# Optimization experiments

Measured on AMD Instinct MI355X. Metric: run time of the kernel, lower is better.

Reference implementation:

```python
import jax, jax.numpy as jnp
import numpy as np

EPS = 1e-6     # torch F.pairwise_distance eps (added to the difference)
MARGIN = 1.0


def setup_inputs() -> dict:
    key = jax.random.key(0)
    k1, k2, k3 = jax.random.split(key, 3)
    dim = 2400
    anchor = jax.random.normal(k1, (1, dim), dtype=jnp.float32)
    positive_samples = jax.random.normal(k2, (5, dim), dtype=jnp.float32)
    negative_samples = jax.random.normal(k3, (50000, dim), dtype=jnp.float32)
    return {"anchor": anchor, "positive_samples": positive_samples,
            "negative_samples": negative_samples}


def reference(anchor, positive_samples, negative_samples):
    # Faithful to the torch loop: TripletMarginLoss(margin=1.0, p=2, swap=False,
    # reduction='sum') applied to each chunk of num_pos negatives, summed.
    # d(x, y) = ||x - y + eps||_2  (torch pairwise_distance semantics)
    P = positive_samples.shape[0]            # 5 personas
    N = negative_samples.shape[0]
    C = N // P                               # number of full chunks (partial dropped)
    # anchor broadcasts (1, D) against (P, D)
    d_ap = jnp.sqrt(jnp.sum(jnp.square(anchor - positive_samples + EPS), axis=-1))  # (P,)
    neg = negative_samples[: C * P].reshape(C, P, -1)                               # (C, P, D)
    d_an = jnp.sqrt(jnp.sum(jnp.square(anchor[None] - neg + EPS), axis=-1))         # (C, P)
    loss = jnp.sum(jax.nn.relu(d_ap[None, :] - d_an + MARGIN))
    return loss
```

## Files before the change

### kernel.cpp

```cpp
#include <hip/hip_runtime.h>
#include <math.h>

#define DIM 2400
#define VEC (DIM / 4)
#define EPS 1e-6f
#define MARGIN 1.0f
#define NPOS 5

__global__ void dap_kernel(const float* __restrict__ anchor,
                           const float* __restrict__ pos,
                           float* __restrict__ dap,
                           float* __restrict__ out) {
    const int lane = threadIdx.x & 63;
    const int wave = threadIdx.x >> 6;
    const float4* a4 = (const float4*)anchor;
    const float4* p4 = (const float4*)(pos + wave * DIM);

    float acc = 0.0f;
    for (int w = lane; w < VEC; w += 64) {
        float4 a = a4[w];
        float4 b = p4[w];
        float dx = a.x - b.x + EPS;
        float dy = a.y - b.y + EPS;
        float dz = a.z - b.z + EPS;
        float dw = a.w - b.w + EPS;
        acc = fmaf(dx, dx, fmaf(dy, dy, fmaf(dz, dz, fmaf(dw, dw, acc))));
    }
    #pragma unroll
    for (int off = 32; off > 0; off >>= 1)
        acc += __shfl_down(acc, off, 64);
    if (lane == 0) dap[wave] = sqrtf(acc);
    if (threadIdx.x == 0) *out = 0.0f;
}

__global__ __launch_bounds__(256, 4)
void triplet_kernel(const float* __restrict__ anchor,
                    const float* __restrict__ neg,
                    const float* __restrict__ dap,
                    float* __restrict__ out,
                    int n_rows) {
    __shared__ float4 s_anchor[VEC];
    __shared__ float  s_dap[NPOS];
    __shared__ float  s_partial[4];

    for (int i = threadIdx.x; i < VEC; i += blockDim.x)
        s_anchor[i] = ((const float4*)anchor)[i];
    if (threadIdx.x < NPOS)
        s_dap[threadIdx.x] = dap[threadIdx.x];
    __syncthreads();

    const int lane = threadIdx.x & 63;
    const int wave = threadIdx.x >> 6;
    const int waves_per_block = blockDim.x >> 6;
    const int stride = gridDim.x * waves_per_block;

    float local = 0.0f;
    for (int row = blockIdx.x * waves_per_block + wave; row < n_rows; row += stride) {
        const float4* nr = (const float4*)(neg + (size_t)row * DIM);
        float acc = 0.0f;
        #pragma unroll 3
        for (int w = lane; w < VEC; w += 64) {
            float4 a = s_anchor[w];
            float4 b = nr[w];
            float dx = a.x - b.x + EPS;
            float dy = a.y - b.y + EPS;
            float dz = a.z - b.z + EPS;
            float dw = a.w - b.w + EPS;
            acc = fmaf(dx, dx, fmaf(dy, dy, fmaf(dz, dz, fmaf(dw, dw, acc))));
        }
        #pragma unroll
        for (int off = 32; off > 0; off >>= 1)
            acc += __shfl_down(acc, off, 64);
        if (lane == 0) {
            float d_an = sqrtf(acc);
            float t = s_dap[row % NPOS] - d_an + MARGIN;
            local += fmaxf(t, 0.0f);
        }
    }

    if (lane == 0) s_partial[wave] = local;
    __syncthreads();
    if (threadIdx.x == 0) {
        float blocksum = 0.0f;
        for (int w = 0; w < waves_per_block; ++w) blocksum += s_partial[w];
        atomicAdd(out, blocksum);
    }
}

extern "C" void kernel_launch(void* const* d_in, const int* in_sizes, int n_in,
                              void* d_out, int out_size, void* d_ws, size_t ws_size,
                              hipStream_t stream) {
    const float* anchor = (const float*)d_in[0];
    const float* pos    = (const float*)d_in[1];
    const float* neg    = (const float*)d_in[2];
    float* out = (float*)d_out;
    float* dap = (float*)d_ws;

    const int n_neg  = in_sizes[2] / DIM;
    const int n_rows = (n_neg / NPOS) * NPOS;

    dap_kernel<<<1, NPOS * 64, 0, stream>>>(anchor, pos, dap, out);

    const int block = 256;
    const int waves_per_block = block / 64;
    int grid = 2048;
    int max_grid = (n_rows + waves_per_block - 1) / waves_per_block;
    if (grid > max_grid) grid = max_grid;
    triplet_kernel<<<grid, block, 0, stream>>>(anchor, neg, dap, out, n_rows);
}
```

Before: 623.7 us.

## Process two rows per wave with all loads issued upfront for memory-level parallelism

Each wave now handles a pair of negative rows and issues all of their float4 loads (10 per lane per row) into registers before doing any arithmetic. Out-of-range lanes are clamped and masked to zero. The goal is more outstanding memory requests per wave, to better saturate HBM bandwidth on this streaming reduction. The grid is halved to match, and register pressure rises to 80 float4 values per lane, which may reduce occupancy under launch_bounds(256,4).

```diff
diff --git a/kernel.cpp b/kernel.cpp
--- a/kernel.cpp
+++ b/kernel.cpp
@@ -2,10 +2,11 @@
 #include <math.h>
 
 #define DIM 2400
-#define VEC (DIM / 4)
+#define VEC 600
 #define EPS 1e-6f
 #define MARGIN 1.0f
 #define NPOS 5
+#define NLOAD 10
 
 __global__ void dap_kernel(const float* __restrict__ anchor,
                            const float* __restrict__ pos,
@@ -49,32 +50,61 @@
         s_dap[threadIdx.x] = dap[threadIdx.x];
     __syncthreads();
 
-    const int lane = threadIdx.x & 63;
-    const int wave = threadIdx.x >> 6;
-    const int waves_per_block = blockDim.x >> 6;
-    const int stride = gridDim.x * waves_per_block;
+    const int lane   = threadIdx.x & 63;
+    const int wave   = threadIdx.x >> 6;
+    const int wpb    = blockDim.x >> 6;
+    const int gwave  = blockIdx.x * wpb + wave;
+    const int nwaves = gridDim.x * wpb;
+    const int npairs = (n_rows + 1) >> 1;
 
     float local = 0.0f;
-    for (int row = blockIdx.x * waves_per_block + wave; row < n_rows; row += stride) {
-        const float4* nr = (const float4*)(neg + (size_t)row * DIM);
-        float acc = 0.0f;
-        #pragma unroll 3
-        for (int w = lane; w < VEC; w += 64) {
-            float4 a = s_anchor[w];
-            float4 b = nr[w];
-            float dx = a.x - b.x + EPS;
-            float dy = a.y - b.y + EPS;
-            float dz = a.z - b.z + EPS;
-            float dw = a.w - b.w + EPS;
-            acc = fmaf(dx, dx, fmaf(dy, dy, fmaf(dz, dz, fmaf(dw, dw, acc))));
+    for (int pair = gwave; pair < npairs; pair += nwaves) {
+        const int r0 = pair * 2;
+        const int r1 = r0 + 1;
+        const bool has1 = (r1 < n_rows);
+        const float4* p0 = (const float4*)(neg + (size_t)r0 * DIM);
+        const float4* p1 = (const float4*)(neg + (size_t)(has1 ? r1 : r0) * DIM);
+
+        float4 b0[NLOAD], b1[NLOAD];
+        #pragma unroll
+        for (int k = 0; k < NLOAD; ++k) {
+            int w  = lane + 64 * k;
+            int wc = (w < VEC) ? w : lane;
+            b0[k] = p0[wc];
+            b1[k] = p1[wc];
         }
+
+        float acc0 = 0.0f, acc1 = 0.0f;
         #pragma unroll
-        for (int off = 32; off > 0; off >>= 1)
-            acc += __shfl_down(acc, off, 64);
+        for (int k = 0; k < NLOAD; ++k) {
+            int w  = lane + 64 * k;
+            bool v = (w < VEC);
+            float4 a = s_anchor[v ? w : lane];
+            float m  = v ? 1.0f : 0.0f;
+            float dx0 = (a.x - b0[k].x + EPS) * m;
+            float dy0 = (a.y - b0[k].y + EPS) * m;
+            float dz0 = (a.z - b0[k].z + EPS) * m;
+            float dw0 = (a.w - b0[k].w + EPS) * m;
+            acc0 = fmaf(dx0, dx0, fmaf(dy0, dy0, fmaf(dz0, dz0, fmaf(dw0, dw0, acc0))));
+            float dx1 = (a.x - b1[k].x + EPS) * m;
+            float dy1 = (a.y - b1[k].y + EPS) * m;
+            float dz1 = (a.z - b1[k].z + EPS) * m;
+            float dw1 = (a.w - b1[k].w + EPS) * m;
+            acc1 = fmaf(dx1, dx1, fmaf(dy1, dy1, fmaf(dz1, dz1, fmaf(dw1, dw1, acc1))));
+        }
+
+        #pragma unroll
+        for (int off = 32; off > 0; off >>= 1) {
+            acc0 += __shfl_xor(acc0, off, 64);
+            acc1 += __shfl_xor(acc1, off, 64);
+        }
         if (lane == 0) {
-            float d_an = sqrtf(acc);
-            float t = s_dap[row % NPOS] - d_an + MARGIN;
-            local += fmaxf(t, 0.0f);
+            float t0 = s_dap[r0 % NPOS] - sqrtf(acc0) + MARGIN;
+            local += fmaxf(t0, 0.0f);
+            if (has1) {
+                float t1 = s_dap[r1 % NPOS] - sqrtf(acc1) + MARGIN;
+                local += fmaxf(t1, 0.0f);
+            }
         }
     }
 
@@ -82,7 +112,7 @@
     __syncthreads();
     if (threadIdx.x == 0) {
         float blocksum = 0.0f;
-        for (int w = 0; w < waves_per_block; ++w) blocksum += s_partial[w];
+        for (int w = 0; w < wpb; ++w) blocksum += s_partial[w];
         atomicAdd(out, blocksum);
     }
 }
@@ -102,9 +132,10 @@
     dap_kernel<<<1, NPOS * 64, 0, stream>>>(anchor, pos, dap, out);
 
     const int block = 256;
-    const int waves_per_block = block / 64;
-    int grid = 2048;
-    int max_grid = (n_rows + waves_per_block - 1) / waves_per_block;
+    const int wpb = block / 64;
+    const int npairs = (n_rows + 1) / 2;
+    int grid = 1024;
+    int max_grid = (npairs + wpb - 1) / wpb;
     if (grid > max_grid) grid = max_grid;
     triplet_kernel<<<grid, block, 0, stream>>>(anchor, neg, dap, out, n_rows);
 }
```

Result: slower. 646.8 us (+3.7%).

## Double-buffer negative rows into LDS via global_load_lds with single-wave blocks

Applied to the files above, without the earlier changes.

Restructures the triplet kernel so each 64-thread block streams one negative row at a time into LDS using async global-to-LDS DMA, prefetching the next row while computing the current one. The anchor is kept in registers and dap values in registers, removing shared anchor reads and the block-level reduction. Relies on hand-encoded s_waitcnt values and fewer total waves, risking lower memory parallelism or subtle ordering bugs.

```diff
diff --git a/kernel.cpp b/kernel.cpp
--- a/kernel.cpp
+++ b/kernel.cpp
@@ -1,11 +1,13 @@
 #include <hip/hip_runtime.h>
 #include <math.h>
+#include <stdint.h>
 
 #define DIM 2400
-#define VEC (DIM / 4)
+#define VEC 600
 #define EPS 1e-6f
 #define MARGIN 1.0f
 #define NPOS 5
+#define NLOAD 10
 
 __global__ void dap_kernel(const float* __restrict__ anchor,
                            const float* __restrict__ pos,
@@ -33,58 +35,88 @@
     if (threadIdx.x == 0) *out = 0.0f;
 }
 
-__global__ __launch_bounds__(256, 4)
+__device__ __forceinline__ void dma_row(const float4* __restrict__ grow,
+                                        float4* lbuf, int lane) {
+    #pragma unroll
+    for (int i = 0; i < 9; ++i) {
+        const float4* g = grow + i * 64 + lane;
+        float4* l = lbuf + i * 64;
+        __builtin_amdgcn_global_load_lds(
+            (const __attribute__((address_space(1))) void*)g,
+            (__attribute__((address_space(3))) void*)l, 16, 0, 0);
+    }
+    if (lane < 24) {
+        const float4* g = grow + 576 + lane;
+        float4* l = lbuf + 576;
+        __builtin_amdgcn_global_load_lds(
+            (const __attribute__((address_space(1))) void*)g,
+            (__attribute__((address_space(3))) void*)l, 16, 0, 0);
+    }
+}
+
+__global__ __launch_bounds__(64)
 void triplet_kernel(const float* __restrict__ anchor,
                     const float* __restrict__ neg,
                     const float* __restrict__ dap,
                     float* __restrict__ out,
                     int n_rows) {
-    __shared__ float4 s_anchor[VEC];
-    __shared__ float  s_dap[NPOS];
-    __shared__ float  s_partial[4];
+    __shared__ float4 sbuf[2][VEC];
 
-    for (int i = threadIdx.x; i < VEC; i += blockDim.x)
-        s_anchor[i] = ((const float4*)anchor)[i];
-    if (threadIdx.x < NPOS)
-        s_dap[threadIdx.x] = dap[threadIdx.x];
-    __syncthreads();
+    const int lane = threadIdx.x;
+    const int nw   = gridDim.x;
 
-    const int lane = threadIdx.x & 63;
-    const int wave = threadIdx.x >> 6;
-    const int waves_per_block = blockDim.x >> 6;
-    const int stride = gridDim.x * waves_per_block;
+    float4 areg[NLOAD];
+    const float4* a4 = (const float4*)anchor;
+    #pragma unroll
+    for (int k = 0; k < NLOAD; ++k) {
+        int idx = k * 64 + lane;
+        areg[k] = a4[idx < VEC ? idx : VEC - 1];
+    }
+    float dv[NPOS];
+    #pragma unroll
+    for (int p = 0; p < NPOS; ++p) dv[p] = dap[p];
 
     float local = 0.0f;
-    for (int row = blockIdx.x * waves_per_block + wave; row < n_rows; row += stride) {
-        const float4* nr = (const float4*)(neg + (size_t)row * DIM);
-        float acc = 0.0f;
-        #pragma unroll 3
-        for (int w = lane; w < VEC; w += 64) {
-            float4 a = s_anchor[w];
-            float4 b = nr[w];
-            float dx = a.x - b.x + EPS;
-            float dy = a.y - b.y + EPS;
-            float dz = a.z - b.z + EPS;
-            float dw = a.w - b.w + EPS;
-            acc = fmaf(dx, dx, fmaf(dy, dy, fmaf(dz, dz, fmaf(dw, dw, acc))));
-        }
-        #pragma unroll
-        for (int off = 32; off > 0; off >>= 1)
-            acc += __shfl_down(acc, off, 64);
-        if (lane == 0) {
-            float d_an = sqrtf(acc);
-            float t = s_dap[row % NPOS] - d_an + MARGIN;
-            local += fmaxf(t, 0.0f);
+    int r = blockIdx.x;
+    if (r < n_rows) {
+        int cur = 0;
+        dma_row((const float4*)(neg + (size_t)r * DIM), sbuf[0], lane);
+        while (true) {
+            const int rn = r + nw;
+            const bool have_next = (rn < n_rows);
+            if (have_next)
+                dma_row((const float4*)(neg + (size_t)rn * DIM), sbuf[cur ^ 1], lane);
+
+            if (have_next) __builtin_amdgcn_s_waitcnt(0x0F7A);
+            else           __builtin_amdgcn_s_waitcnt(0x0F70);
+
+            const float4* lb = sbuf[cur];
+            float acc = 0.0f;
+            #pragma unroll
+            for (int k = 0; k < NLOAD; ++k) {
+                int idx = k * 64 + lane;
+                int ci  = (idx < VEC) ? idx : VEC - 1;
+                float m = (idx < VEC) ? 1.0f : 0.0f;
+                float4 b = lb[ci];
+                float4 a = areg[k];
+                float dx = (a.x - b.x + EPS) * m;
+                float dy = (a.y - b.y + EPS) * m;
+                float dz = (a.z - b.z + EPS) * m;
+                float dw = (a.w - b.w + EPS) * m;
+                acc = fmaf(dx, dx, fmaf(dy, dy, fmaf(dz, dz, fmaf(dw, dw, acc))));
+            }
+            #pragma unroll
+            for (int off = 32; off > 0; off >>= 1)
+                acc += __shfl_xor(acc, off, 64);
+            if (lane == 0)
+                local += fmaxf(dv[r % NPOS] - sqrtf(acc) + MARGIN, 0.0f);
+
+            if (!have_next) break;
+            r = rn;
+            cur ^= 1;
         }
     }
-
-    if (lane == 0) s_partial[wave] = local;
-    __syncthreads();
-    if (threadIdx.x == 0) {
-        float blocksum = 0.0f;
-        for (int w = 0; w < waves_per_block; ++w) blocksum += s_partial[w];
-        atomicAdd(out, blocksum);
-    }
+    if (lane == 0) atomicAdd(out, local);
 }
 
 extern "C" void kernel_launch(void* const* d_in, const int* in_sizes, int n_in,
@@ -101,10 +133,7 @@
 
     dap_kernel<<<1, NPOS * 64, 0, stream>>>(anchor, pos, dap, out);
 
-    const int block = 256;
-    const int waves_per_block = block / 64;
     int grid = 2048;
-    int max_grid = (n_rows + waves_per_block - 1) / waves_per_block;
-    if (grid > max_grid) grid = max_grid;
-    triplet_kernel<<<grid, block, 0, stream>>>(anchor, neg, dap, out, n_rows);
+    if (grid > n_rows) grid = n_rows;
+    triplet_kernel<<<grid, 64, 0, stream>>>(anchor, neg, dap, out, n_rows);
 }
```

After: 625.1 us. Within noise of the previous version (+0.2%).
